# Optimization experiments

Hardware: AMD Instinct MI355X
Metric: run time of the kernel (lower is better)

## Reference

```python
import jax, jax.numpy as jnp
import numpy as np

N = 100000
D = 128
E = 1600000
NEG_SLOPE = 0.2


def gatv2_layer(x, src, dst, Wl, Wr, att, b):
    # GATv2Conv (heads=1, eval mode): lin_l -> source/message feats, lin_r -> target feats
    xl = x @ Wl                      # [N, D]
    xr = x @ Wr                      # [N, D]
    # per-edge score: a^T LeakyReLU(x_l[src] + x_r[dst])
    z = jax.nn.leaky_relu(xl[src] + xr[dst], NEG_SLOPE)  # [E, D]
    e = z @ att                      # [E]
    # segment softmax over incoming edges of each dst node
    m = jax.ops.segment_max(e, dst, num_segments=N)      # [N]
    ex = jnp.exp(e - m[dst])
    s = jax.ops.segment_sum(ex, dst, num_segments=N)     # [N]
    alpha = ex / (s[dst] + 1e-16)                        # [E]
    # weighted scatter-aggregate of source messages
    out = jax.ops.segment_sum(alpha[:, None] * xl[src], dst, num_segments=N)
    return out + b


def setup_inputs() -> dict:
    key = jax.random.key(0)
    ks = jax.random.split(key, 6)
    scale = 1.0 / np.sqrt(D)
    x = jax.random.normal(ks[0], (N, D), dtype=jnp.float32)
    edge_index = jax.random.randint(ks[1], (2, E), 0, N, dtype=jnp.int64)
    Wl = jax.random.normal(ks[2], (3, D, D), dtype=jnp.float32) * scale
    Wr = jax.random.normal(ks[3], (3, D, D), dtype=jnp.float32) * scale
    att = jax.random.normal(ks[4], (3, D), dtype=jnp.float32) * scale
    b = jax.random.normal(ks[5], (3, D), dtype=jnp.float32) * 0.01
    return {"x": x, "Wl": Wl, "Wr": Wr, "att": att, "b": b, "edge_index": edge_index}


def reference(x, Wl, Wr, att, b, edge_index):
    src, dst = edge_index[0], edge_index[1]
    h = gatv2_layer(x, src, dst, Wl[0], Wr[0], att[0], b[0])
    h = jax.nn.relu(h)
    h = gatv2_layer(h, src, dst, Wl[1], Wr[1], att[1], b[1])
    h = jax.nn.relu(h)
    h = gatv2_layer(h, src, dst, Wl[2], Wr[2], att[2], b[2])
    return h
```

## Files before the change

kernel.cpp:

```cpp
#include <hip/hip_runtime.h>
#include <math.h>

#define DD 128
#define NEG 0.2f

typedef short short8 __attribute__((ext_vector_type(8)));
typedef float f32x4 __attribute__((ext_vector_type(4)));
typedef float f32x2 __attribute__((ext_vector_type(2)));
typedef _Float16 h2v __attribute__((ext_vector_type(2)));

__device__ __forceinline__ unsigned short f2bf(float f) {
    unsigned u = __float_as_uint(f);
    return (unsigned short)((u + 0x7fffu + ((u >> 16) & 1u)) >> 16);
}
__device__ __forceinline__ float bf2f(unsigned short h) {
    return __uint_as_float(((unsigned)h) << 16);
}

#if __has_builtin(__builtin_amdgcn_exp2f)
#define EXP2F(x) __builtin_amdgcn_exp2f(x)
#else
#define EXP2F(x) exp2f(x)
#endif

__device__ void excl_scan_1024(int* sh, int* aux) {
    __syncthreads();
    int t = threadIdx.x;
    int base = t * 4;
    int a0 = sh[base], a1 = sh[base + 1], a2 = sh[base + 2], a3 = sh[base + 3];
    int s = a0 + a1 + a2 + a3;
    aux[t] = s;
    __syncthreads();
    for (int off = 1; off < 256; off <<= 1) {
        int v = (t >= off) ? aux[t - off] : 0;
        __syncthreads();
        aux[t] += v;
        __syncthreads();
    }
    int excl = aux[t] - s;
    sh[base] = excl;
    sh[base + 1] = excl + a0;
    sh[base + 2] = excl + a0 + a1;
    sh[base + 3] = excl + a0 + a1 + a2;
    __syncthreads();
}

__global__ __launch_bounds__(256) void k_histC(const int* __restrict__ dst,
                                               int* __restrict__ histC, int E, int CB) {
    __shared__ int h[1024];
    int t = threadIdx.x;
    for (int j = t; j < 1024; j += 256) h[j] = 0;
    __syncthreads();
    int stride = gridDim.x * 256;
    for (int i = blockIdx.x * 256 + t; i < E; i += stride)
        atomicAdd(&h[dst[i] >> 7], 1);
    __syncthreads();
    for (int j = t; j < CB; j += 256)
        if (h[j]) atomicAdd(&histC[j], h[j]);
}

__global__ __launch_bounds__(256) void k_scanC2(const int* __restrict__ histC,
                                                int* __restrict__ baseC,
                                                int* __restrict__ cursorC, int CB) {
    __shared__ int sh[1024];
    __shared__ int aux[256];
    int t = threadIdx.x;
    for (int j = t; j < 1024; j += 256) sh[j] = (j < CB) ? histC[j] : 0;
    excl_scan_1024(sh, aux);
    for (int j = t; j <= CB; j += 256) {
        baseC[j] = sh[j];
        if (j < CB) cursorC[j] = sh[j];
    }
}

#define CHUNK 8192
__global__ __launch_bounds__(256) void k_part3(const int* __restrict__ srcI,
                                               const int* __restrict__ dstI,
                                               int* __restrict__ cursorC,
                                               uint2* __restrict__ part,
                                               int E, int CB) {
    __shared__ int sh[1024];
    __shared__ int aux[256];
    __shared__ int resBase[1024];
    __shared__ int cur[1024];
    __shared__ uint2 stage[CHUNK];
    int t = threadIdx.x;
    int c0 = blockIdx.x * CHUNK;
    int cnt = E - c0; if (cnt > CHUNK) cnt = CHUNK;

    for (int j = t; j < 1024; j += 256) sh[j] = 0;
    __syncthreads();
    for (int i = t; i < cnt; i += 256)
        atomicAdd(&sh[dstI[c0 + i] >> 7], 1);
    __syncthreads();
    for (int j = t; j < CB; j += 256) {
        int c = sh[j];
        resBase[j] = c ? atomicAdd(&cursorC[j], c) : 0;
    }
    excl_scan_1024(sh, aux);
    for (int j = t; j < 1024; j += 256) cur[j] = sh[j];
    __syncthreads();
    for (int i = t; i < cnt; i += 256) {
        unsigned s = (unsigned)srcI[c0 + i];
        unsigned d = (unsigned)dstI[c0 + i];
        int b = (int)(d >> 7);
        int pos = atomicAdd(&cur[b], 1);
        stage[pos].x = s;
        stage[pos].y = d;
    }
    __syncthreads();
    for (int i = t; i < cnt; i += 256) {
        uint2 v = stage[i];
        int b = (int)(v.y >> 7);
        part[resBase[b] + (i - sh[b])] = v;
    }
}

__global__ __launch_bounds__(256) void k_part4(const uint2* __restrict__ part,
                                               const int* __restrict__ baseC,
                                               int* __restrict__ srcs,
                                               int* __restrict__ row_ptr,
                                               int N) {
    __shared__ int hist[128];
    __shared__ int incl[128];
    __shared__ int cur[128];
    __shared__ unsigned srcS[8192];
    int b = blockIdx.x;
    int t = threadIdx.x;
    int base = baseC[b];
    int cnt = baseC[b + 1] - base;
    int node0 = b << 7;

    if (t < 128) hist[t] = 0;
    __syncthreads();
    for (int i = t; i < cnt; i += 256)
        atomicAdd(&hist[part[base + i].y & 127], 1);
    __syncthreads();
    if (t < 128) incl[t] = hist[t];
    __syncthreads();
    for (int off = 1; off < 128; off <<= 1) {
        int v = 0;
        if (t < 128 && t >= off) v = incl[t - off];
        __syncthreads();
        if (t < 128) incl[t] += v;
        __syncthreads();
    }
    if (t < 128) cur[t] = incl[t] - hist[t];
    __syncthreads();
    for (int i = t; i < cnt; i += 256) {
        uint2 e = part[base + i];
        int r = atomicAdd(&cur[e.y & 127], 1);
        if (r < 8192) srcS[r] = e.x;
    }
    __syncthreads();
    for (int i = t; i < cnt; i += 256)
        srcs[base + i] = (int)srcS[i];
    int nodes = N - node0; if (nodes > 128) nodes = 128;
    if (t < nodes) row_ptr[node0 + t + 1] = base + incl[t];
    if (b == 0 && t == 0) row_ptr[0] = 0;
}

#define NCH 8192
__global__ __launch_bounds__(256) void k_deghist(const int* __restrict__ row_ptr,
                                                 int* __restrict__ histD, int N) {
    __shared__ int h[128];
    int t = threadIdx.x;
    if (t < 128) h[t] = 0;
    __syncthreads();
    int c0 = blockIdx.x * NCH;
    int cnt = N - c0; if (cnt > NCH) cnt = NCH;
    for (int i = t; i < cnt; i += 256) {
        int deg = row_ptr[c0 + i + 1] - row_ptr[c0 + i];
        int c = deg < 127 ? deg : 127;
        atomicAdd(&h[c], 1);
    }
    __syncthreads();
    if (t < 128 && h[t]) atomicAdd(&histD[t], h[t]);
}

__global__ __launch_bounds__(128) void k_degscan(const int* __restrict__ histD,
                                                 int* __restrict__ cursorD) {
    __shared__ int sh[128];
    int t = threadIdx.x;
    int v0 = histD[t];
    sh[t] = v0;
    __syncthreads();
    for (int off = 1; off < 128; off <<= 1) {
        int v = (t >= off) ? sh[t - off] : 0;
        __syncthreads();
        sh[t] += v;
        __syncthreads();
    }
    cursorD[t] = sh[t] - v0;
}

__global__ __launch_bounds__(256) void k_degpart(const int* __restrict__ row_ptr,
                                                 int* __restrict__ cursorD,
                                                 int* __restrict__ order, int N) {
    __shared__ int hist[128];
    __shared__ int excl[128];
    __shared__ int cur[128];
    __shared__ int resB[128];
    __shared__ int stage[NCH];
    int t = threadIdx.x;
    int c0 = blockIdx.x * NCH;
    int cnt = N - c0; if (cnt > NCH) cnt = NCH;

    if (t < 128) hist[t] = 0;
    __syncthreads();
    for (int i = t; i < cnt; i += 256) {
        int deg = row_ptr[c0 + i + 1] - row_ptr[c0 + i];
        int c = deg < 127 ? deg : 127;
        atomicAdd(&hist[c], 1);
    }
    __syncthreads();
    if (t < 128) resB[t] = hist[t] ? atomicAdd(&cursorD[t], hist[t]) : 0;
    if (t < 128) excl[t] = hist[t];
    __syncthreads();
    for (int off = 1; off < 128; off <<= 1) {
        int v = 0;
        if (t < 128 && t >= off) v = excl[t - off];
        __syncthreads();
        if (t < 128) excl[t] += v;
        __syncthreads();
    }
    if (t < 128) { excl[t] -= hist[t]; cur[t] = excl[t]; }
    __syncthreads();
    for (int i = t; i < cnt; i += 256) {
        int deg = row_ptr[c0 + i + 1] - row_ptr[c0 + i];
        int c = deg < 127 ? deg : 127;
        int p = atomicAdd(&cur[c], 1);
        stage[p] = (c << 20) | (c0 + i);
    }
    __syncthreads();
    for (int i = t; i < cnt; i += 256) {
        int v = stage[i];
        int c = v >> 20;
        order[resB[c] + (i - excl[c])] = v & 0xFFFFF;
    }
}

__global__ void k_castx(const float* __restrict__ x, unsigned short* __restrict__ hi,
                        unsigned short* __restrict__ lo, int n) {
    int i = (blockIdx.x * blockDim.x + threadIdx.x) * 4;
    if (i >= n) return;
    float4 v = *(const float4*)(x + i);
    unsigned short h[4], l[4];
    float f[4] = {v.x, v.y, v.z, v.w};
#pragma unroll
    for (int j = 0; j < 4; j++) {
        h[j] = f2bf(f[j]);
        l[j] = f2bf(f[j] - bf2f(h[j]));
    }
    *(uint2*)(hi + i) = *(uint2*)h;
    *(uint2*)(lo + i) = *(uint2*)l;
}

__global__ void k_castw(const float* __restrict__ Wl, const float* __restrict__ Wr,
                        unsigned short* __restrict__ Wth, unsigned short* __restrict__ Wtl) {
    int idx = blockIdx.x * blockDim.x + threadIdx.x;
    if (idx >= 3 * 256 * 128) return;
    int L = idx >> 15;
    int rem = idx & 32767;
    int nn = rem >> 7;
    int k = rem & 127;
    float v = (nn < 128) ? Wl[L * 16384 + k * 128 + nn]
                         : Wr[L * 16384 + k * 128 + (nn - 128)];
    unsigned short h = f2bf(v);
    Wth[idx] = h;
    Wtl[idx] = f2bf(v - bf2f(h));
}

__global__ __launch_bounds__(256) void k_gemm(const unsigned short* __restrict__ Ahi,
                                              const unsigned short* __restrict__ Alo,
                                              const unsigned short* __restrict__ Wth,
                                              const unsigned short* __restrict__ Wtl,
                                              _Float16* __restrict__ xl, _Float16* __restrict__ xr,
                                              int M, int L) {
    __shared__ unsigned short sA[2][128][40];
    __shared__ unsigned short sB[2][128][40];
    int t = threadIdx.x;
    int lane = t & 63;
    int l15 = lane & 15;
    int quad = lane >> 4;
    int wave = t >> 6;
    int wm = wave & 1;
    int wn = wave >> 1;
    int r0 = blockIdx.x * 128;
    const unsigned short* WthL = Wth + ((size_t)L * 256 + blockIdx.y * 128) * 128;
    const unsigned short* WtlL = Wtl + ((size_t)L * 256 + blockIdx.y * 128) * 128;

    f32x4 acc[4][4] = {};

    for (int kc = 0; kc < 4; kc++) {
        int k0 = kc * 32;
        if (kc) __syncthreads();
#pragma unroll
        for (int i = 0; i < 2; i++) {
            int s = t + i * 256;
            int row = s >> 2;
            int kq = (s & 3) * 8;
            int gr = r0 + row; gr = gr < M ? gr : M - 1;
            uint2 va0 = *(const uint2*)(Ahi + (size_t)gr * DD + k0 + kq);
            uint2 va1 = *(const uint2*)(Ahi + (size_t)gr * DD + k0 + kq + 4);
            *(uint2*)&sA[0][row][kq] = va0;
            *(uint2*)&sA[0][row][kq + 4] = va1;
            uint2 vb0 = *(const uint2*)(Alo + (size_t)gr * DD + k0 + kq);
            uint2 vb1 = *(const uint2*)(Alo + (size_t)gr * DD + k0 + kq + 4);
            *(uint2*)&sA[1][row][kq] = vb0;
            *(uint2*)&sA[1][row][kq + 4] = vb1;
            uint2 wa0 = *(const uint2*)(WthL + (size_t)row * DD + k0 + kq);
            uint2 wa1 = *(const uint2*)(WthL + (size_t)row * DD + k0 + kq + 4);
            *(uint2*)&sB[0][row][kq] = wa0;
            *(uint2*)&sB[0][row][kq + 4] = wa1;
            uint2 wb0 = *(const uint2*)(WtlL + (size_t)row * DD + k0 + kq);
            uint2 wb1 = *(const uint2*)(WtlL + (size_t)row * DD + k0 + kq + 4);
            *(uint2*)&sB[1][row][kq] = wb0;
            *(uint2*)&sB[1][row][kq + 4] = wb1;
        }
        __syncthreads();

        union F8 { short8 v; uint2 u[2]; };
        F8 ah[4], al[4], bh[4], bl[4];
#pragma unroll
        for (int mt = 0; mt < 4; mt++) {
            const unsigned short* p = &sA[0][wm * 64 + mt * 16 + l15][quad * 8];
            ah[mt].u[0] = *(const uint2*)p; ah[mt].u[1] = *(const uint2*)(p + 4);
            const unsigned short* q = &sA[1][wm * 64 + mt * 16 + l15][quad * 8];
            al[mt].u[0] = *(const uint2*)q; al[mt].u[1] = *(const uint2*)(q + 4);
        }
#pragma unroll
        for (int nt = 0; nt < 4; nt++) {
            const unsigned short* p = &sB[0][wn * 64 + nt * 16 + l15][quad * 8];
            bh[nt].u[0] = *(const uint2*)p; bh[nt].u[1] = *(const uint2*)(p + 4);
            const unsigned short* q = &sB[1][wn * 64 + nt * 16 + l15][quad * 8];
            bl[nt].u[0] = *(const uint2*)q; bl[nt].u[1] = *(const uint2*)(q + 4);
        }
#pragma unroll
        for (int mt = 0; mt < 4; mt++)
#pragma unroll
            for (int nt = 0; nt < 4; nt++) {
                acc[mt][nt] = __builtin_amdgcn_mfma_f32_16x16x32_bf16(ah[mt].v, bh[nt].v, acc[mt][nt], 0, 0, 0);
                acc[mt][nt] = __builtin_amdgcn_mfma_f32_16x16x32_bf16(al[mt].v, bh[nt].v, acc[mt][nt], 0, 0, 0);
                acc[mt][nt] = __builtin_amdgcn_mfma_f32_16x16x32_bf16(ah[mt].v, bl[nt].v, acc[mt][nt], 0, 0, 0);
            }
    }

    _Float16* C = blockIdx.y ? xr : xl;
#pragma unroll
    for (int mt = 0; mt < 4; mt++)
#pragma unroll
        for (int r = 0; r < 4; r++) {
            int row = r0 + wm * 64 + mt * 16 + quad * 4 + r;
            if (row < M) {
#pragma unroll
                for (int nt = 0; nt < 4; nt++)
                    C[(size_t)row * DD + wn * 64 + nt * 16 + l15] = (_Float16)acc[mt][nt][r];
            }
        }
}

__global__ __launch_bounds__(256) void k_attn(const _Float16* __restrict__ xl,
                                              const _Float16* __restrict__ xr,
                                              const int* __restrict__ row_ptr,
                                              const int* __restrict__ srcs,
                                              const int* __restrict__ order,
                                              const float* __restrict__ att,
                                              const float* __restrict__ bias,
                                              float* __restrict__ outF,
                                              unsigned short* __restrict__ outHi,
                                              unsigned short* __restrict__ outLo,
                                              int n, int mode) {
    int wid = (blockIdx.x * blockDim.x + threadIdx.x) >> 6;
    int l = threadIdx.x & 63;
    int l15 = l & 15;
    int g = l >> 4;
    int idx = wid * 4 + g;
    bool act = idx < n;
    int d = act ? order[idx] : 0;

    union Q { uint4 q; h2v h[4]; };
    const float LOG2E = 1.44269504088896f;

    h2v at[4], xrh[4];
    {
        float4 a0 = *(const float4*)(att + l15 * 8);
        float4 a1 = *(const float4*)(att + l15 * 8 + 4);
        at[0] = h2v{(_Float16)(a0.x * LOG2E), (_Float16)(a0.y * LOG2E)};
        at[1] = h2v{(_Float16)(a0.z * LOG2E), (_Float16)(a0.w * LOG2E)};
        at[2] = h2v{(_Float16)(a1.x * LOG2E), (_Float16)(a1.y * LOG2E)};
        at[3] = h2v{(_Float16)(a1.z * LOG2E), (_Float16)(a1.w * LOG2E)};
        Q hr; hr.q = *(const uint4*)(xr + (size_t)d * DD + l15 * 8);
#pragma unroll
        for (int j = 0; j < 4; j++) xrh[j] = hr.h[j];
    }
    const _Float16 cneg = (_Float16)NEG;

    int beg = act ? row_ptr[d] : 0;
    int end = act ? row_ptr[d + 1] : 0;
    int cnt = end - beg;

    int mc = cnt;
    mc = max(mc, __shfl_xor(mc, 16, 64));
    mc = max(mc, __shfl_xor(mc, 32, 64));
    int iters = (mc + 1) >> 1;

    float lse = 0.f;
    float av[8] = {};

    int i0 = beg, i1 = beg + 1;
    bool v0 = i0 < end, v1 = i1 < end;
    int s0 = v0 ? srcs[i0] : 0;
    int s1 = v1 ? srcs[i1] : 0;

    const _Float16* xlp = xl + l15 * 8;

    for (int it = 0; it < iters; ++it) {
        Q h0, h1;
        h0.q = *(const uint4*)(xlp + (size_t)s0 * DD);
        h1.q = *(const uint4*)(xlp + (size_t)s1 * DD);
        int n0 = i0 + 2, n1 = i1 + 2;
        bool nv0 = n0 < end, nv1 = n1 < end;
        int t0 = nv0 ? srcs[n0] : 0;
        int t1 = nv1 ? srcs[n1] : 0;

        float p0 = 0.f, p1 = 0.f;
#pragma unroll
        for (int j = 0; j < 4; j++) {
            h2v z0 = h0.h[j] + xrh[j];
            h2v zl0 = __builtin_elementwise_max(z0, z0 * cneg);
            p0 = __builtin_amdgcn_fdot2(zl0, at[j], p0, false);
            h2v z1 = h1.h[j] + xrh[j];
            h2v zl1 = __builtin_elementwise_max(z1, z1 * cneg);
            p1 = __builtin_amdgcn_fdot2(zl1, at[j], p1, false);
        }
        p0 += __shfl_xor(p0, 1, 64);  p1 += __shfl_xor(p1, 1, 64);
        p0 += __shfl_xor(p0, 2, 64);  p1 += __shfl_xor(p1, 2, 64);
        p0 += __shfl_xor(p0, 4, 64);  p1 += __shfl_xor(p1, 4, 64);
        p0 += __shfl_xor(p0, 8, 64);  p1 += __shfl_xor(p1, 8, 64);
        p0 = fminf(fmaxf(p0, -86.f), 86.f);
        p1 = fminf(fmaxf(p1, -86.f), 86.f);
        float w0 = v0 ? EXP2F(p0) : 0.f;
        float w1 = v1 ? EXP2F(p1) : 0.f;
        lse += w0 + w1;
#pragma unroll
        for (int j = 0; j < 4; j++) {
            av[2 * j]     += (float)h0.h[j][0] * w0;
            av[2 * j + 1] += (float)h0.h[j][1] * w0;
            av[2 * j]     += (float)h1.h[j][0] * w1;
            av[2 * j + 1] += (float)h1.h[j][1] * w1;
        }
        i0 = n0; i1 = n1; v0 = nv0; v1 = nv1; s0 = t0; s1 = t1;
    }

    if (act) {
        float inv = (cnt > 0) ? 1.0f / lse : 0.f;
        float o[8];
        float4 b0 = *(const float4*)(bias + l15 * 8);
        float4 b1 = *(const float4*)(bias + l15 * 8 + 4);
        float bv[8] = {b0.x, b0.y, b0.z, b0.w, b1.x, b1.y, b1.z, b1.w};
#pragma unroll
        for (int j = 0; j < 8; j++) o[j] = av[j] * inv + bv[j];
        if (mode) {
            union U8 { unsigned short s[8]; uint4 q; };
            U8 hh, ll;
#pragma unroll
            for (int j = 0; j < 8; j++) {
                float v = fmaxf(o[j], 0.f);
                hh.s[j] = f2bf(v);
                ll.s[j] = f2bf(v - bf2f(hh.s[j]));
            }
            *(uint4*)(outHi + (size_t)d * DD + l15 * 8) = hh.q;
            *(uint4*)(outLo + (size_t)d * DD + l15 * 8) = ll.q;
        } else {
            float4 o0 = {o[0], o[1], o[2], o[3]};
            float4 o1 = {o[4], o[5], o[6], o[7]};
            float* op = outF + (size_t)d * DD + l15 * 8;
            *(float4*)op = o0;
            *(float4*)(op + 4) = o1;
        }
    }
}

extern "C" void kernel_launch(void* const* d_in, const int* in_sizes, int n_in,
                              void* d_out, int out_size, void* d_ws, size_t ws_size,
                              hipStream_t stream) {
    const float* x    = (const float*)d_in[0];
    const float* Wl   = (const float*)d_in[1];
    const float* Wr   = (const float*)d_in[2];
    const float* att  = (const float*)d_in[3];
    const float* bias = (const float*)d_in[4];
    const int*   ei   = (const int*)d_in[5];

    int N = in_sizes[0] / DD;
    int E = in_sizes[5] / 2;
    const int* srcI = ei;
    const int* dstI = ei + E;
    float* out = (float*)d_out;
    int CB = (N + 127) >> 7;

    char* ws = (char*)d_ws;
    size_t off = 0;
    auto alloc = [&](size_t bytes) -> void* {
        void* p = ws + off;
        off += (bytes + 255) & ~(size_t)255;
        return p;
    };
    _Float16*       xl   = (_Float16*)alloc((size_t)N * DD * 2);
    _Float16*       xr   = (_Float16*)alloc((size_t)N * DD * 2);
    unsigned short* Ahi  = (unsigned short*)alloc((size_t)N * DD * 2);
    unsigned short* Alo  = (unsigned short*)alloc((size_t)N * DD * 2);
    unsigned short* Wth  = (unsigned short*)alloc((size_t)3 * 256 * 128 * 2);
    unsigned short* Wtl  = (unsigned short*)alloc((size_t)3 * 256 * 128 * 2);
    uint2* part    = (uint2*)alloc((size_t)E * 8);
    int*   srcs    = (int*)alloc((size_t)E * 4);
    int*   row_ptr = (int*)alloc((size_t)(N + 1) * 4);
    int*   order   = (int*)alloc((size_t)N * 4);
    int*   histC   = (int*)alloc((size_t)(CB + 1) * 4);
    int*   baseC   = (int*)alloc((size_t)(CB + 1) * 4);
    int*   cursorC = (int*)alloc((size_t)(CB + 1) * 4);
    int*   histD   = (int*)alloc(128 * 4);
    int*   cursorD = (int*)alloc(128 * 4);

    const int tb = 256;
    (void)hipMemsetAsync(histC, 0, (size_t)CB * 4, stream);
    (void)hipMemsetAsync(histD, 0, 128 * 4, stream);
    k_histC<<<256, 256, 0, stream>>>(dstI, histC, E, CB);
    k_scanC2<<<1, 256, 0, stream>>>(histC, baseC, cursorC, CB);
    k_part3<<<(E + CHUNK - 1) / CHUNK, 256, 0, stream>>>(srcI, dstI, cursorC, part, E, CB);
    k_part4<<<CB, 256, 0, stream>>>(part, baseC, srcs, row_ptr, N);
    int gD = (N + NCH - 1) / NCH;
    k_deghist<<<gD, 256, 0, stream>>>(row_ptr, histD, N);
    k_degscan<<<1, 128, 0, stream>>>(histD, cursorD);
    k_degpart<<<gD, 256, 0, stream>>>(row_ptr, cursorD, order, N);

    k_castw<<<(3 * 256 * 128 + tb - 1) / tb, tb, 0, stream>>>(Wl, Wr, Wth, Wtl);
    k_castx<<<((size_t)N * DD / 4 + tb - 1) / tb, tb, 0, stream>>>(x, Ahi, Alo, N * DD);

    int gX = (N + 127) / 128;
    for (int L = 0; L < 3; ++L) {
        k_gemm<<<dim3(gX, 2), 256, 0, stream>>>(Ahi, Alo, Wth, Wtl, xl, xr, N, L);
        k_attn<<<((size_t)N * 16 + tb - 1) / tb, tb, 0, stream>>>(
            xl, xr, row_ptr, srcs, order, att + (size_t)L * DD, bias + (size_t)L * DD,
            out, Ahi, Alo, N, (L < 2) ? 1 : 0);
    }
}
```

Before: 510.0 us.

## Load GEMM fragments directly from global and unroll attention edge loop by four

The GEMM kernel drops its shared-memory staging and barriers. Each wave now loads its MFMA operand fragments straight from global memory, and one 512-thread block computes both the xl and xr column halves so the A rows are read by a single block. Separately, the attention kernel handles four edges per iteration instead of two, which puts more independent gathers in flight to hide memory latency. The trade-offs are redundant global loads across waves that rely on the cache, and higher register pressure in both kernels.

Result: slower. 609.1 us (+19.4%).

```diff
diff --git a/kernel.cpp b/kernel.cpp
--- a/kernel.cpp
+++ b/kernel.cpp
@@ -271,70 +271,52 @@
     Wtl[idx] = f2bf(v - bf2f(h));
 }
 
-__global__ __launch_bounds__(256) void k_gemm(const unsigned short* __restrict__ Ahi,
-                                              const unsigned short* __restrict__ Alo,
-                                              const unsigned short* __restrict__ Wth,
-                                              const unsigned short* __restrict__ Wtl,
-                                              _Float16* __restrict__ xl, _Float16* __restrict__ xr,
-                                              int M, int L) {
-    __shared__ unsigned short sA[2][128][40];
-    __shared__ unsigned short sB[2][128][40];
+__global__ __launch_bounds__(512, 2) void k_gemm(const unsigned short* __restrict__ Ahi,
+                                                 const unsigned short* __restrict__ Alo,
+                                                 const unsigned short* __restrict__ Wth,
+                                                 const unsigned short* __restrict__ Wtl,
+                                                 _Float16* __restrict__ xl, _Float16* __restrict__ xr,
+                                                 int M, int L) {
     int t = threadIdx.x;
     int lane = t & 63;
     int l15 = lane & 15;
     int quad = lane >> 4;
-    int wave = t >> 6;
-    int wm = wave & 1;
-    int wn = wave >> 1;
+    int w = t >> 6;
+    int wm = w >> 2;
+    int wn = w & 3;
     int r0 = blockIdx.x * 128;
-    const unsigned short* WthL = Wth + ((size_t)L * 256 + blockIdx.y * 128) * 128;
-    const unsigned short* WtlL = Wtl + ((size_t)L * 256 + blockIdx.y * 128) * 128;
+    const unsigned short* WthL = Wth + (size_t)L * 256 * 128;
+    const unsigned short* WtlL = Wtl + (size_t)L * 256 * 128;
+
+    size_t offA[4], offB[4];
+#pragma unroll
+    for (int mt = 0; mt < 4; mt++) {
+        int r = r0 + wm * 64 + mt * 16 + l15;
+        r = r < M ? r : M - 1;
+        offA[mt] = (size_t)r * DD + quad * 8;
+    }
+#pragma unroll
+    for (int nt = 0; nt < 4; nt++) {
+        int c = wn * 64 + nt * 16 + l15;
+        offB[nt] = (size_t)c * DD + quad * 8;
+    }
 
     f32x4 acc[4][4] = {};
-
+    union F8 { short8 v; uint4 u; };
+
+#pragma unroll
     for (int kc = 0; kc < 4; kc++) {
         int k0 = kc * 32;
-        if (kc) __syncthreads();
-#pragma unroll
-        for (int i = 0; i < 2; i++) {
-            int s = t + i * 256;
-            int row = s >> 2;
-            int kq = (s & 3) * 8;
-            int gr = r0 + row; gr = gr < M ? gr : M - 1;
-            uint2 va0 = *(const uint2*)(Ahi + (size_t)gr * DD + k0 + kq);
-            uint2 va1 = *(const uint2*)(Ahi + (size_t)gr * DD + k0 + kq + 4);
-            *(uint2*)&sA[0][row][kq] = va0;
-            *(uint2*)&sA[0][row][kq + 4] = va1;
-            uint2 vb0 = *(const uint2*)(Alo + (size_t)gr * DD + k0 + kq);
-            uint2 vb1 = *(const uint2*)(Alo + (size_t)gr * DD + k0 + kq + 4);
-            *(uint2*)&sA[1][row][kq] = vb0;
-            *(uint2*)&sA[1][row][kq + 4] = vb1;
-            uint2 wa0 = *(const uint2*)(WthL + (size_t)row * DD + k0 + kq);
-            uint2 wa1 = *(const uint2*)(WthL + (size_t)row * DD + k0 + kq + 4);
-            *(uint2*)&sB[0][row][kq] = wa0;
-            *(uint2*)&sB[0][row][kq + 4] = wa1;
-            uint2 wb0 = *(const uint2*)(WtlL + (size_t)row * DD + k0 + kq);
-            uint2 wb1 = *(const uint2*)(WtlL + (size_t)row * DD + k0 + kq + 4);
-            *(uint2*)&sB[1][row][kq] = wb0;
-            *(uint2*)&sB[1][row][kq + 4] = wb1;
+        F8 ah[4], al[4], bh[4], bl[4];
+#pragma unroll
+        for (int mt = 0; mt < 4; mt++) {
+            ah[mt].u = *(const uint4*)(Ahi + offA[mt] + k0);
+            al[mt].u = *(const uint4*)(Alo + offA[mt] + k0);
         }
-        __syncthreads();
-
-        union F8 { short8 v; uint2 u[2]; };
-        F8 ah[4], al[4], bh[4], bl[4];
-#pragma unroll
-        for (int mt = 0; mt < 4; mt++) {
-            const unsigned short* p = &sA[0][wm * 64 + mt * 16 + l15][quad * 8];
-            ah[mt].u[0] = *(const uint2*)p; ah[mt].u[1] = *(const uint2*)(p + 4);
-            const unsigned short* q = &sA[1][wm * 64 + mt * 16 + l15][quad * 8];
-            al[mt].u[0] = *(const uint2*)q; al[mt].u[1] = *(const uint2*)(q + 4);
-        }
 #pragma unroll
         for (int nt = 0; nt < 4; nt++) {
-            const unsigned short* p = &sB[0][wn * 64 + nt * 16 + l15][quad * 8];
-            bh[nt].u[0] = *(const uint2*)p; bh[nt].u[1] = *(const uint2*)(p + 4);
-            const unsigned short* q = &sB[1][wn * 64 + nt * 16 + l15][quad * 8];
-            bl[nt].u[0] = *(const uint2*)q; bl[nt].u[1] = *(const uint2*)(q + 4);
+            bh[nt].u = *(const uint4*)(WthL + offB[nt] + k0);
+            bl[nt].u = *(const uint4*)(WtlL + offB[nt] + k0);
         }
 #pragma unroll
         for (int mt = 0; mt < 4; mt++)
@@ -346,7 +328,6 @@
             }
     }
 
-    _Float16* C = blockIdx.y ? xr : xl;
 #pragma unroll
     for (int mt = 0; mt < 4; mt++)
 #pragma unroll
@@ -354,8 +335,11 @@
             int row = r0 + wm * 64 + mt * 16 + quad * 4 + r;
             if (row < M) {
 #pragma unroll
-                for (int nt = 0; nt < 4; nt++)
-                    C[(size_t)row * DD + wn * 64 + nt * 16 + l15] = (_Float16)acc[mt][nt][r];
+                for (int nt = 0; nt < 4; nt++) {
+                    int col = wn * 64 + nt * 16 + l15;
+                    _Float16* C = (col < 128) ? xl : xr;
+                    C[(size_t)row * DD + (col & 127)] = (_Float16)acc[mt][nt][r];
+                }
             }
         }
 }
@@ -403,28 +387,34 @@
     int mc = cnt;
     mc = max(mc, __shfl_xor(mc, 16, 64));
     mc = max(mc, __shfl_xor(mc, 32, 64));
-    int iters = (mc + 1) >> 1;
+    int iters = (mc + 3) >> 2;
 
     float lse = 0.f;
     float av[8] = {};
 
-    int i0 = beg, i1 = beg + 1;
-    bool v0 = i0 < end, v1 = i1 < end;
+    int i0 = beg, i1 = beg + 1, i2 = beg + 2, i3 = beg + 3;
+    bool v0 = i0 < end, v1 = i1 < end, v2 = i2 < end, v3 = i3 < end;
     int s0 = v0 ? srcs[i0] : 0;
     int s1 = v1 ? srcs[i1] : 0;
+    int s2 = v2 ? srcs[i2] : 0;
+    int s3 = v3 ? srcs[i3] : 0;
 
     const _Float16* xlp = xl + l15 * 8;
 
     for (int it = 0; it < iters; ++it) {
-        Q h0, h1;
+        Q h0, h1, h2, h3;
         h0.q = *(const uint4*)(xlp + (size_t)s0 * DD);
         h1.q = *(const uint4*)(xlp + (size_t)s1 * DD);
-        int n0 = i0 + 2, n1 = i1 + 2;
-        bool nv0 = n0 < end, nv1 = n1 < end;
+        h2.q = *(const uint4*)(xlp + (size_t)s2 * DD);
+        h3.q = *(const uint4*)(xlp + (size_t)s3 * DD);
+        int n0 = i0 + 4, n1 = i1 + 4, n2 = i2 + 4, n3 = i3 + 4;
+        bool nv0 = n0 < end, nv1 = n1 < end, nv2 = n2 < end, nv3 = n3 < end;
         int t0 = nv0 ? srcs[n0] : 0;
         int t1 = nv1 ? srcs[n1] : 0;
-
-        float p0 = 0.f, p1 = 0.f;
+        int t2 = nv2 ? srcs[n2] : 0;
+        int t3 = nv3 ? srcs[n3] : 0;
+
+        float p0 = 0.f, p1 = 0.f, p2 = 0.f, p3 = 0.f;
 #pragma unroll
         for (int j = 0; j < 4; j++) {
             h2v z0 = h0.h[j] + xrh[j];
@@ -433,24 +423,44 @@
             h2v z1 = h1.h[j] + xrh[j];
             h2v zl1 = __builtin_elementwise_max(z1, z1 * cneg);
             p1 = __builtin_amdgcn_fdot2(zl1, at[j], p1, false);
+            h2v z2 = h2.h[j] + xrh[j];
+            h2v zl2 = __builtin_elementwise_max(z2, z2 * cneg);
+            p2 = __builtin_amdgcn_fdot2(zl2, at[j], p2, false);
+            h2v z3 = h3.h[j] + xrh[j];
+            h2v zl3 = __builtin_elementwise_max(z3, z3 * cneg);
+            p3 = __builtin_amdgcn_fdot2(zl3, at[j], p3, false);
         }
         p0 += __shfl_xor(p0, 1, 64);  p1 += __shfl_xor(p1, 1, 64);
+        p2 += __shfl_xor(p2, 1, 64);  p3 += __shfl_xor(p3, 1, 64);
         p0 += __shfl_xor(p0, 2, 64);  p1 += __shfl_xor(p1, 2, 64);
+        p2 += __shfl_xor(p2, 2, 64);  p3 += __shfl_xor(p3, 2, 64);
         p0 += __shfl_xor(p0, 4, 64);  p1 += __shfl_xor(p1, 4, 64);
+        p2 += __shfl_xor(p2, 4, 64);  p3 += __shfl_xor(p3, 4, 64);
         p0 += __shfl_xor(p0, 8, 64);  p1 += __shfl_xor(p1, 8, 64);
+        p2 += __shfl_xor(p2, 8, 64);  p3 += __shfl_xor(p3, 8, 64);
         p0 = fminf(fmaxf(p0, -86.f), 86.f);
         p1 = fminf(fmaxf(p1, -86.f), 86.f);
+        p2 = fminf(fmaxf(p2, -86.f), 86.f);
+        p3 = fminf(fmaxf(p3, -86.f), 86.f);
         float w0 = v0 ? EXP2F(p0) : 0.f;
         float w1 = v1 ? EXP2F(p1) : 0.f;
-        lse += w0 + w1;
+        float w2 = v2 ? EXP2F(p2) : 0.f;
+        float w3 = v3 ? EXP2F(p3) : 0.f;
+        lse += (w0 + w1) + (w2 + w3);
 #pragma unroll
         for (int j = 0; j < 4; j++) {
             av[2 * j]     += (float)h0.h[j][0] * w0;
             av[2 * j + 1] += (float)h0.h[j][1] * w0;
             av[2 * j]     += (float)h1.h[j][0] * w1;
             av[2 * j + 1] += (float)h1.h[j][1] * w1;
+            av[2 * j]     += (float)h2.h[j][0] * w2;
+            av[2 * j + 1] += (float)h2.h[j][1] * w2;
+            av[2 * j]     += (float)h3.h[j][0] * w3;
+            av[2 * j + 1] += (float)h3.h[j][1] * w3;
         }
-        i0 = n0; i1 = n1; v0 = nv0; v1 = nv1; s0 = t0; s1 = t1;
+        i0 = n0; i1 = n1; i2 = n2; i3 = n3;
+        v0 = nv0; v1 = nv1; v2 = nv2; v3 = nv3;
+        s0 = t0; s1 = t1; s2 = t2; s3 = t3;
     }
 
     if (act) {
@@ -539,7 +549,7 @@
 
     int gX = (N + 127) / 128;
     for (int L = 0; L < 3; ++L) {
-        k_gemm<<<dim3(gX, 2), 256, 0, stream>>>(Ahi, Alo, Wth, Wtl, xl, xr, N, L);
+        k_gemm<<<gX, 512, 0, stream>>>(Ahi, Alo, Wth, Wtl, xl, xr, N, L);
         k_attn<<<((size_t)N * 16 + tb - 1) / tb, tb, 0, stream>>>(
             xl, xr, row_ptr, srcs, order, att + (size_t)L * DD, bias + (size_t)L * DD,
             out, Ahi, Alo, N, (L < 2) ? 1 : 0);
```
